# Performance work log

Hardware: AMD Instinct MI355X
Metric: run time of the kernel (lower is better)

## Reference

```python
import jax
import jax.numpy as jnp
import numpy as np
from jax import lax

IOU_THRESH = 0.5
TOP, LEFT, BOTTOM, RIGHT = 0, 1, 2, 3


def setup_inputs() -> dict:
    key = jax.random.key(0)
    k1, k2, k3, k4, k5 = jax.random.split(key, 5)
    B, N, C = 4, 3000, 21
    # plausible boxes in (top, left, bottom, right) with positive height/width
    tl = jax.random.uniform(k1, (B, N, 2), dtype=jnp.float32) * 800.0
    wh = jax.random.uniform(k2, (B, N, 2), dtype=jnp.float32) * 200.0 + 1.0
    nms_reg = jnp.concatenate([tl, tl + wh], axis=2)
    nms_cls = jax.random.normal(k3, (B, N, 1), dtype=jnp.float32)
    rcnn_reg = jax.random.normal(k4, (B, N, 4), dtype=jnp.float32) * 2.0
    rcnn_cls = jax.random.normal(k5, (B, N, C), dtype=jnp.float32)
    return {"nms_reg": nms_reg, "nms_cls": nms_cls,
            "rcnn_reg": rcnn_reg, "rcnn_cls": rcnn_cls, "reduction": 16}


def _pairwise_iou(boxes):
    # boxes: [N, 4] in (top, left, bottom, right). IoU is invariant to the
    # (x, y) axis permutation the original applies before torchvision.nms.
    t, l, b, r = boxes[:, 0], boxes[:, 1], boxes[:, 2], boxes[:, 3]
    area = jnp.maximum(b - t, 0.0) * jnp.maximum(r - l, 0.0)  # [N]
    ih = jnp.maximum(jnp.minimum(b[:, None], b[None, :]) - jnp.maximum(t[:, None], t[None, :]), 0.0)
    iw = jnp.maximum(jnp.minimum(r[:, None], r[None, :]) - jnp.maximum(l[:, None], l[None, :]), 0.0)
    inter = ih * iw  # [N, N]
    union = area[:, None] + area[None, :] - inter
    return inter / jnp.maximum(union, 1e-9)


def _nms_keep(iou, scores):
    # Greedy NMS over one class. iou: [N, N]; scores: [N] (-inf = not this class).
    # Matches torchvision.ops.nms: suppress boxes with IoU > threshold.
    N = scores.shape[0]
    idx = jnp.arange(N)

    def step(state, _):
        rem, keep = state
        i = jnp.argmax(rem)
        valid = rem[i] > -jnp.inf
        keep = keep.at[i].set(valid)
        suppress = (iou[i] > IOU_THRESH) | (idx == i)
        rem = jnp.where(valid & suppress, -jnp.inf, rem)
        return (rem, keep), None

    (_, keep), _ = lax.scan(step, (scores, jnp.zeros(N, dtype=bool)), None, length=N)
    return keep


def reference(nms_reg, nms_cls, rcnn_reg, rcnn_cls, reduction):
    red = jnp.float32(reduction)
    # round top/left down, bottom/right up on the feature grid, back to pixels
    nms_reg_rounded = jnp.concatenate(
        [jnp.floor(nms_reg[:, :, :2] * red), jnp.ceil(nms_reg[:, :, 2:] * red)],
        axis=2) / red
    # rcnn_reg[:, :, c] += nms_reg_rounded[:, :, c] for all 4 coords
    boxes = rcnn_reg + nms_reg_rounded  # [B, N, 4]
    probs = jax.nn.softmax(rcnn_cls, axis=2)  # [B, N, C]
    nms_cls_sig = jax.nn.sigmoid(nms_cls)

    amax = jnp.argmax(probs, axis=2)  # [B, N]
    C = probs.shape[2]
    class_ids = jnp.arange(1, C)  # skip background class 0
    # per-class masked scores: [B, C-1, N]
    cls_scores = jnp.transpose(probs, (0, 2, 1))[:, 1:, :]
    scores = jnp.where(amax[:, None, :] == class_ids[None, :, None],
                       cls_scores, -jnp.inf)

    iou = jax.vmap(_pairwise_iou)(boxes)  # [B, N, N] (shared across classes)
    keep_per_class = jax.vmap(lambda io, sc: jax.vmap(lambda s: _nms_keep(io, s))(sc))(iou, scores)  # [B, C-1, N]
    keep = jnp.any(keep_per_class, axis=1)  # [B, N]; argmax classes are disjoint

    return (nms_reg_rounded, nms_cls_sig, boxes, probs, keep)
```

## Files before the change

kernel.cpp:

```cpp
#include <hip/hip_runtime.h>
#include <cfloat>
#include <climits>

#define B 4
#define N 3000
#define C 21
#define SORT_N 256
#define WORDS 4
#define NMS_BLOCKS (B * (C - 1))
#define PW_BLOCKS 12
#define TPB 1024


__device__ __forceinline__ int softmax_am(const float* __restrict__ lg,
                                          float* __restrict__ pmax_out,
                                          float* __restrict__ pstore) {
    float m = lg[0];
    #pragma unroll
    for (int c = 1; c < C; ++c) m = fmaxf(m, lg[c]);
    float p[C];
    float sum = 0.0f;
    #pragma unroll
    for (int c = 0; c < C; ++c) {
        p[c] = expf(__fsub_rn(lg[c], m));
        sum = __fadd_rn(sum, p[c]);
    }
    float best = -1.0f; int bc = 0;
    #pragma unroll
    for (int c = 0; c < C; ++c) {
        float pc = __fdiv_rn(p[c], sum);
        if (pstore) pstore[c] = pc;
        if (pc > best) { best = pc; bc = c; }
    }
    *pmax_out = best;
    return bc;
}

__device__ __forceinline__ void make_boxes(float4 nr, float4 rr, float red,
                                           float4* rounded, float4* box) {
    float r0 = floorf(__fmul_rn(nr.x, red)) / red;
    float r1 = floorf(__fmul_rn(nr.y, red)) / red;
    float r2 = ceilf (__fmul_rn(nr.z, red)) / red;
    float r3 = ceilf (__fmul_rn(nr.w, red)) / red;
    *rounded = make_float4(r0, r1, r2, r3);
    *box = make_float4(__fadd_rn(rr.x, r0), __fadd_rn(rr.y, r1),
                       __fadd_rn(rr.z, r2), __fadd_rn(rr.w, r3));
}

__global__ __launch_bounds__(TPB) void fused_kernel(
    const float* __restrict__ nms_reg,
    const float* __restrict__ nms_cls,
    const float* __restrict__ rcnn_reg,
    const float* __restrict__ rcnn_cls,
    const int* __restrict__ red_p,
    float* __restrict__ out)
{
    const int tid = threadIdx.x;

    float* out_round = out;
    float* out_sig   = out + B * N * 4;
    float* out_boxes = out + B * N * 5;
    float* out_probs = out + B * N * 9;
    float* out_keep  = out + B * N * 30;

    if (blockIdx.x >= NMS_BLOCKS) {
        const int bn = (blockIdx.x - NMS_BLOCKS) * TPB + tid;
        if (bn >= B * N) return;

        float red = (float)(*red_p);

        float4 nr = ((const float4*)nms_reg)[bn];
        float4 rr = ((const float4*)rcnn_reg)[bn];
        float4 rounded, box;
        make_boxes(nr, rr, red, &rounded, &box);
        ((float4*)out_round)[bn] = rounded;
        ((float4*)out_boxes)[bn] = box;

        float x = nms_cls[bn];
        float s;
        if (x >= 0.0f) s = 1.0f / (1.0f + expf(-x));
        else { float e = expf(x); s = e / (1.0f + e); }
        out_sig[bn] = s;

        float pm;
        int am = softmax_am(rcnn_cls + (size_t)bn * C, &pm, out_probs + (size_t)bn * C);

        if (am == 0) out_keep[bn] = 0.0f;
        return;
    }

    const int b = blockIdx.x / (C - 1);
    const int c = blockIdx.x % (C - 1) + 1;
    const int lane = tid & 63;

    __shared__ int   gid[SORT_N];
    __shared__ float gsc[SORT_N];
    __shared__ int   rnk[SORT_N];
    __shared__ int   sid[SORT_N];
    __shared__ float bt[SORT_N], bl[SORT_N], bb[SORT_N], br_[SORT_N], ar[SORT_N];
    __shared__ __align__(16) unsigned long long msk[SORT_N][WORDS];
    __shared__ unsigned long long aout[WORDS];
    __shared__ int mcount;

    if (tid == 0) mcount = 0;
    if (tid < SORT_N) rnk[tid] = 0;
    __syncthreads();

    #pragma unroll
    for (int chunk = 0; chunk < 3; ++chunk) {
        int n = chunk * TPB + tid;
        bool match = false;
        float pm = 0.0f;
        if (n < N) {
            int am = softmax_am(rcnn_cls + (size_t)(b * N + n) * C, &pm, nullptr);
            match = (am == c);
        }
        unsigned long long mb = __ballot(match);
        int base = 0;
        if (lane == 0 && mb) base = atomicAdd(&mcount, __popcll(mb));
        base = __shfl(base, 0);
        if (match) {
            int pos = base + __popcll(mb & ((1ull << lane) - 1ull));
            if (pos < SORT_N) { gid[pos] = n; gsc[pos] = pm; }
        }
    }
    __syncthreads();
    const int M = min(mcount, SORT_N);

    {
        int e = tid & 255, q = tid >> 8;
        if (e < M) {
            float mys = gsc[e]; int myi = gid[e];
            int j0 = q * 64, j1 = min(j0 + 64, M);
            int partial = 0;
            for (int j = j0; j < j1; ++j) {
                float sj = gsc[j]; int ij = gid[j];
                partial += ((sj > mys) || (sj == mys && ij < myi)) ? 1 : 0;
            }
            if (partial) atomicAdd(&rnk[e], partial);
        }
    }
    __syncthreads();

    if (tid < M) {
        float red = (float)(*red_p);
        int n = gid[tid];
        int rank = rnk[tid];
        float4 nr = ((const float4*)nms_reg)[b * N + n];
        float4 rr = ((const float4*)rcnn_reg)[b * N + n];
        float4 rounded, box;
        make_boxes(nr, rr, red, &rounded, &box);
        sid[rank] = n;
        bt[rank] = box.x; bl[rank] = box.y; bb[rank] = box.z; br_[rank] = box.w;
        ar[rank] = __fmul_rn(fmaxf(__fsub_rn(box.z, box.x), 0.0f),
                             fmaxf(__fsub_rn(box.w, box.y), 0.0f));
    }
    __syncthreads();

    {
        int g = tid >> 8;
        int j = tid & 255;
        int w = (tid >> 6) & 3;
        float jt = 0.f, jl = 0.f, jb = 0.f, jr = 0.f, ja = 0.f;
        if (j < M) { jt = bt[j]; jl = bl[j]; jb = bb[j]; jr = br_[j]; ja = ar[j]; }
        int r0 = g * 64, r1 = min(r0 + 64, M);
        const double THR = 0.5 + 0x1p-25;
        for (int r = r0; r < r1; ++r) {
            float rt = bt[r], rl = bl[r], rb = bb[r], rr2 = br_[r], ra = ar[r];
            bool supp = false;
            if (j > r && j < M) {
                float ih = fmaxf(__fsub_rn(fminf(rb, jb), fmaxf(rt, jt)), 0.0f);
                float iw = fmaxf(__fsub_rn(fminf(rr2, jr), fmaxf(rl, jl)), 0.0f);
                float inter = __fmul_rn(ih, iw);
                float uni = __fsub_rn(__fadd_rn(ra, ja), inter);
                float den = fmaxf(uni, 1e-9f);
                supp = ((double)inter > (double)den * THR);
            }
            unsigned long long wm = __ballot(supp);
            if (lane == 0) msk[r][w] = wm;
        }
    }
    __syncthreads();

    if (tid < 64) {
        auto onesk = [](int k) -> unsigned long long {
            return k <= 0 ? 0ull : (k >= 64 ? ~0ull : ((1ull << k) - 1ull));
        };
        unsigned long long a0 = onesk(M), a1 = onesk(M - 64), a2 = onesk(M - 128), a3 = onesk(M - 192);
        {
            int e = min(64, M);
            #pragma unroll 4
            for (int i = 0; i < e; ++i) {
                unsigned long long sel = 0ull - ((a0 >> i) & 1ull);
                a0 &= ~(msk[i][0] & sel);
                a1 &= ~(msk[i][1] & sel);
                a2 &= ~(msk[i][2] & sel);
                a3 &= ~(msk[i][3] & sel);
            }
        }
        {
            int e = min(128, M);
            #pragma unroll 4
            for (int i = 64; i < e; ++i) {
                unsigned long long sel = 0ull - ((a1 >> (i - 64)) & 1ull);
                a1 &= ~(msk[i][1] & sel);
                a2 &= ~(msk[i][2] & sel);
                a3 &= ~(msk[i][3] & sel);
            }
        }
        {
            int e = min(192, M);
            #pragma unroll 4
            for (int i = 128; i < e; ++i) {
                unsigned long long sel = 0ull - ((a2 >> (i - 128)) & 1ull);
                a2 &= ~(msk[i][2] & sel);
                a3 &= ~(msk[i][3] & sel);
            }
        }
        {
            int e = min(256, M);
            #pragma unroll 4
            for (int i = 192; i < e; ++i) {
                unsigned long long sel = 0ull - ((a3 >> (i - 192)) & 1ull);
                a3 &= ~(msk[i][3] & sel);
            }
        }
        if (lane == 0) { aout[0] = a0; aout[1] = a1; aout[2] = a2; aout[3] = a3; }
    }
    __syncthreads();

    if (tid < M) {
        unsigned long long aw = aout[tid >> 6];
        bool kept = (aw >> (tid & 63)) & 1ull;
        int n = sid[tid];
        out_keep[b * N + n] = (kept && n != 0) ? 1.0f : 0.0f;
    }
}

extern "C" void kernel_launch(void* const* d_in, const int* in_sizes, int n_in,
                              void* d_out, int out_size, void* d_ws, size_t ws_size,
                              hipStream_t stream) {
    const float* nms_reg  = (const float*)d_in[0];
    const float* nms_cls  = (const float*)d_in[1];
    const float* rcnn_reg = (const float*)d_in[2];
    const float* rcnn_cls = (const float*)d_in[3];
    const int*   red_p    = (const int*)d_in[4];
    float* out = (float*)d_out;

    dim3 grid(NMS_BLOCKS + PW_BLOCKS);
    fused_kernel<<<grid, TPB, 0, stream>>>(nms_reg, nms_cls, rcnn_reg, rcnn_cls, red_p, out);
}
```

Before: 102.2 us.

## Split fused kernel into pointwise and NMS kernels sharing argmax via workspace

```diff
diff --git a/kernel.cpp b/kernel.cpp
--- a/kernel.cpp
+++ b/kernel.cpp
@@ -5,36 +5,14 @@
 #define B 4
 #define N 3000
 #define C 21
+#define BN (B * N)
 #define SORT_N 256
 #define WORDS 4
 #define NMS_BLOCKS (B * (C - 1))
-#define PW_BLOCKS 12
-#define TPB 1024
-
-
-__device__ __forceinline__ int softmax_am(const float* __restrict__ lg,
-                                          float* __restrict__ pmax_out,
-                                          float* __restrict__ pstore) {
-    float m = lg[0];
-    #pragma unroll
-    for (int c = 1; c < C; ++c) m = fmaxf(m, lg[c]);
-    float p[C];
-    float sum = 0.0f;
-    #pragma unroll
-    for (int c = 0; c < C; ++c) {
-        p[c] = expf(__fsub_rn(lg[c], m));
-        sum = __fadd_rn(sum, p[c]);
-    }
-    float best = -1.0f; int bc = 0;
-    #pragma unroll
-    for (int c = 0; c < C; ++c) {
-        float pc = __fdiv_rn(p[c], sum);
-        if (pstore) pstore[c] = pc;
-        if (pc > best) { best = pc; bc = c; }
-    }
-    *pmax_out = best;
-    return bc;
-}
+#define PW_TPB 256
+#define PW_GRID ((BN + PW_TPB - 1) / PW_TPB)
+#define NMS_TPB 1024
+
 
 __device__ __forceinline__ void make_boxes(float4 nr, float4 rr, float red,
                                            float4* rounded, float4* box) {
@@ -47,51 +25,77 @@
                        __fadd_rn(rr.z, r2), __fadd_rn(rr.w, r3));
 }
 
-__global__ __launch_bounds__(TPB) void fused_kernel(
+__global__ __launch_bounds__(PW_TPB, 1) void pointwise_kernel(
     const float* __restrict__ nms_reg,
     const float* __restrict__ nms_cls,
     const float* __restrict__ rcnn_reg,
     const float* __restrict__ rcnn_cls,
     const int* __restrict__ red_p,
+    float* __restrict__ out,
+    int* __restrict__ ws_am,
+    float* __restrict__ ws_pm)
+{
+    const int bn = blockIdx.x * PW_TPB + threadIdx.x;
+    if (bn >= BN) return;
+
+    float* out_round = out;
+    float* out_sig   = out + BN * 4;
+    float* out_boxes = out + BN * 5;
+    float* out_probs = out + BN * 9;
+    float* out_keep  = out + BN * 30;
+
+    const float red = (float)(*red_p);
+
+    float4 nr = ((const float4*)nms_reg)[bn];
+    float4 rr = ((const float4*)rcnn_reg)[bn];
+    float4 rounded, box;
+    make_boxes(nr, rr, red, &rounded, &box);
+    ((float4*)out_round)[bn] = rounded;
+    ((float4*)out_boxes)[bn] = box;
+
+    float x = nms_cls[bn];
+    float s;
+    if (x >= 0.0f) s = 1.0f / (1.0f + expf(-x));
+    else { float e = expf(x); s = e / (1.0f + e); }
+    out_sig[bn] = s;
+
+    const float* lg = rcnn_cls + (size_t)bn * C;
+    float m = lg[0];
+    #pragma unroll
+    for (int c = 1; c < C; ++c) m = fmaxf(m, lg[c]);
+    float p[C];
+    float sum = 0.0f;
+    #pragma unroll
+    for (int c = 0; c < C; ++c) {
+        p[c] = expf(__fsub_rn(lg[c], m));
+        sum = __fadd_rn(sum, p[c]);
+    }
+    float best = -1.0f; int bc = 0;
+    float* ps = out_probs + (size_t)bn * C;
+    #pragma unroll
+    for (int c = 0; c < C; ++c) {
+        float pc = __fdiv_rn(p[c], sum);
+        ps[c] = pc;
+        if (pc > best) { best = pc; bc = c; }
+    }
+    ws_am[bn] = bc;
+    ws_pm[bn] = best;
+
+    if (bc == 0) out_keep[bn] = 0.0f;
+}
+
+__global__ __launch_bounds__(NMS_TPB) void nms_kernel(
+    const int* __restrict__ ws_am,
+    const float* __restrict__ ws_pm,
     float* __restrict__ out)
 {
     const int tid = threadIdx.x;
-
-    float* out_round = out;
-    float* out_sig   = out + B * N * 4;
-    float* out_boxes = out + B * N * 5;
-    float* out_probs = out + B * N * 9;
-    float* out_keep  = out + B * N * 30;
-
-    if (blockIdx.x >= NMS_BLOCKS) {
-        const int bn = (blockIdx.x - NMS_BLOCKS) * TPB + tid;
-        if (bn >= B * N) return;
-
-        float red = (float)(*red_p);
-
-        float4 nr = ((const float4*)nms_reg)[bn];
-        float4 rr = ((const float4*)rcnn_reg)[bn];
-        float4 rounded, box;
-        make_boxes(nr, rr, red, &rounded, &box);
-        ((float4*)out_round)[bn] = rounded;
-        ((float4*)out_boxes)[bn] = box;
-
-        float x = nms_cls[bn];
-        float s;
-        if (x >= 0.0f) s = 1.0f / (1.0f + expf(-x));
-        else { float e = expf(x); s = e / (1.0f + e); }
-        out_sig[bn] = s;
-
-        float pm;
-        int am = softmax_am(rcnn_cls + (size_t)bn * C, &pm, out_probs + (size_t)bn * C);
-
-        if (am == 0) out_keep[bn] = 0.0f;
-        return;
-    }
-
     const int b = blockIdx.x / (C - 1);
     const int c = blockIdx.x % (C - 1) + 1;
     const int lane = tid & 63;
+
+    const float* out_boxes = out + BN * 5;
+    float* out_keep        = out + BN * 30;
 
     __shared__ int   gid[SORT_N];
     __shared__ float gsc[SORT_N];
@@ -108,12 +112,12 @@
 
     #pragma unroll
     for (int chunk = 0; chunk < 3; ++chunk) {
-        int n = chunk * TPB + tid;
+        int n = chunk * NMS_TPB + tid;
         bool match = false;
         float pm = 0.0f;
         if (n < N) {
-            int am = softmax_am(rcnn_cls + (size_t)(b * N + n) * C, &pm, nullptr);
-            match = (am == c);
+            match = (ws_am[b * N + n] == c);
+            pm = ws_pm[b * N + n];
         }
         unsigned long long mb = __ballot(match);
         int base = 0;
@@ -143,13 +147,9 @@
     __syncthreads();
 
     if (tid < M) {
-        float red = (float)(*red_p);
         int n = gid[tid];
         int rank = rnk[tid];
-        float4 nr = ((const float4*)nms_reg)[b * N + n];
-        float4 rr = ((const float4*)rcnn_reg)[b * N + n];
-        float4 rounded, box;
-        make_boxes(nr, rr, red, &rounded, &box);
+        float4 box = ((const float4*)out_boxes)[b * N + n];
         sid[rank] = n;
         bt[rank] = box.x; bl[rank] = box.y; bb[rank] = box.z; br_[rank] = box.w;
         ar[rank] = __fmul_rn(fmaxf(__fsub_rn(box.z, box.x), 0.0f),
@@ -247,6 +247,11 @@
     const int*   red_p    = (const int*)d_in[4];
     float* out = (float*)d_out;
 
-    dim3 grid(NMS_BLOCKS + PW_BLOCKS);
-    fused_kernel<<<grid, TPB, 0, stream>>>(nms_reg, nms_cls, rcnn_reg, rcnn_cls, red_p, out);
-}
+    int*   ws_am = (int*)d_ws;
+    float* ws_pm = (float*)((char*)d_ws + BN * sizeof(int));
+
+    pointwise_kernel<<<dim3(PW_GRID), dim3(PW_TPB), 0, stream>>>(
+        nms_reg, nms_cls, rcnn_reg, rcnn_cls, red_p, out, ws_am, ws_pm);
+    nms_kernel<<<dim3(NMS_BLOCKS), dim3(NMS_TPB), 0, stream>>>(
+        ws_am, ws_pm, out);
+}
```

Result: faster. 93.40 us (-8.6%).
